# Kernel tuning notes

Hardware: AMD Instinct MI355X
Metric: run time of the kernel (lower is better)

## Reference

```python
import jax, jax.numpy as jnp
import numpy as np

NPOINT = 1024
NSAMPLE = 32
BN_EPS = 1e-5


def setup_inputs() -> dict:
    key = jax.random.key(0)
    ks = jax.random.split(key, 8)
    B, N, C = 16, 4096, 64
    chans = [C + 3, 64, 64, 128]
    d = {
        "xyz": jax.random.normal(ks[0], (B, N, 3), jnp.float32),
        "points": jax.random.normal(ks[1], (B, N, C), jnp.float32),
    }
    for i in range(3):
        d[f"w{i+1}"] = jax.random.normal(ks[2 + i], (chans[i + 1], chans[i]), jnp.float32) / np.sqrt(chans[i]).astype(np.float32)
        d[f"b{i+1}"] = jnp.zeros((chans[i + 1],), jnp.float32)
        d[f"g{i+1}"] = jnp.ones((chans[i + 1],), jnp.float32)
        d[f"be{i+1}"] = jnp.zeros((chans[i + 1],), jnp.float32)
    return d


def farthest_point_sample(xyz, npoint):
    # xyz: [B, N, 3] -> centroids: [B, npoint] int32 (deterministic start at index 0)
    B, N, _ = xyz.shape

    def step(carry, _):
        distance, farthest = carry
        centroid = jnp.take_along_axis(xyz, farthest[:, None, None], axis=1)  # [B,1,3]
        dist = jnp.sum((xyz - centroid) ** 2, axis=-1)                         # [B,N]
        distance = jnp.minimum(distance, dist)
        new_far = jnp.argmax(distance, axis=-1).astype(jnp.int32)
        return (distance, new_far), farthest

    init = (jnp.full((B, N), 1e10, xyz.dtype), jnp.zeros((B,), jnp.int32))
    _, cents = jax.lax.scan(step, init, None, length=npoint)  # [npoint, B]
    return cents.T  # [B, npoint]


def index_points(points, idx):
    # points: [B,N,C], idx: [B,...] -> [B,...,C]
    return jax.vmap(lambda p, i: p[i])(points, idx)


def bn_relu(h, g, be):
    # training-mode BatchNorm over all axes except channel (last), biased var
    m = h.mean(axis=(0, 1, 2), keepdims=True)
    v = h.var(axis=(0, 1, 2), keepdims=True)
    return jax.nn.relu((h - m) / jnp.sqrt(v + BN_EPS) * g + be)


def reference(xyz, points, w1, b1, g1, be1, w2, b2, g2, be2, w3, b3, g3, be3):
    # --- sample_and_group ---
    fps_idx = farthest_point_sample(xyz, NPOINT)           # [B,S]
    new_xyz = index_points(xyz, fps_idx)                   # [B,S,3]
    # query_ball_point in source ignores radius: kNN via argsort of sq dists
    sqrdists = jnp.sum((new_xyz[:, :, None, :] - xyz[:, None, :, :]) ** 2, axis=-1)  # [B,S,N]
    _, group_idx = jax.lax.top_k(-sqrdists, NSAMPLE)       # [B,S,K] smallest distances
    grouped_xyz = index_points(xyz, group_idx) - new_xyz[:, :, None, :]  # [B,S,K,3]
    grouped_pts = index_points(points, group_idx)          # [B,S,K,C]
    new_points = jnp.concatenate([grouped_xyz, grouped_pts], axis=-1)    # [B,S,K,C+3]
    # --- shared MLP (1x1 conv + BN + ReLU) x3, channel-last layout ---
    h = bn_relu(jnp.einsum("bskc,oc->bsko", new_points, w1) + b1, g1, be1)
    h = bn_relu(jnp.einsum("bskc,oc->bsko", h, w2) + b2, g2, be2)
    h = bn_relu(jnp.einsum("bskc,oc->bsko", h, w3) + b3, g3, be3)
    # max-pool over the neighbor (nsample) axis
    out = jnp.max(h, axis=2)  # [B,S,128]
    return (new_xyz, out)
```

## Files before the change

kernel.cpp:

```cpp
#include <hip/hip_runtime.h>
#include <cstdint>

#define NB   16
#define NPT  4096
#define CINP 64
#define SP   1024
#define KNB  32
#define NROWS (NB*SP*KNB)
#define NT_F  524288.0f
#define NBLK12 4096
#define NBLK3  8192

typedef float v2f __attribute__((ext_vector_type(2)));

__device__ __forceinline__ float sqdist3(float ax, float ay, float az,
                                         float bx, float by, float bz) {
  float dx = ax - bx, dy = ay - by, dz = az - bz;
  return __fadd_rn(__fadd_rn(__fmul_rn(dx, dx), __fmul_rn(dy, dy)), __fmul_rn(dz, dz));
}

#define DPP_STAGE_MAXF(v, ctrl)                                                   \
  do {                                                                            \
    int _t = __builtin_amdgcn_update_dpp(0, __float_as_int(v), ctrl, 0xf, 0xf, false); \
    v = fmaxf(v, __int_as_float(_t));                                             \
  } while (0)

__device__ __forceinline__ float wave_max_f32(float v) {
  DPP_STAGE_MAXF(v, 0x111);
  DPP_STAGE_MAXF(v, 0x112);
  DPP_STAGE_MAXF(v, 0x114);
  DPP_STAGE_MAXF(v, 0x118);
  DPP_STAGE_MAXF(v, 0x142);
  DPP_STAGE_MAXF(v, 0x143);
  return __int_as_float(__builtin_amdgcn_readlane(__float_as_int(v), 63));
}

#define DPP_STAGE_MINU(v, ctrl)                                                   \
  do {                                                                            \
    unsigned _t = (unsigned)__builtin_amdgcn_update_dpp(                          \
        (int)0xFFFFFFFF, (int)(v), ctrl, 0xf, 0xf, false);                        \
    v = (v < _t) ? v : _t;                                                        \
  } while (0)

__device__ __forceinline__ unsigned wave_min_u32(unsigned v) {
  DPP_STAGE_MINU(v, 0x111);
  DPP_STAGE_MINU(v, 0x112);
  DPP_STAGE_MINU(v, 0x114);
  DPP_STAGE_MINU(v, 0x118);
  DPP_STAGE_MINU(v, 0x142);
  DPP_STAGE_MINU(v, 0x143);
  return (unsigned)__builtin_amdgcn_readlane((int)v, 63);
}

#define DPP_STAGE_ADDI(v, ctrl)                                                   \
  do {                                                                            \
    int _t = __builtin_amdgcn_update_dpp(0, (v), ctrl, 0xf, 0xf, false);          \
    v += _t;                                                                      \
  } while (0)

__device__ __forceinline__ int wave_sum_i32(int v) {
  DPP_STAGE_ADDI(v, 0x111);
  DPP_STAGE_ADDI(v, 0x112);
  DPP_STAGE_ADDI(v, 0x114);
  DPP_STAGE_ADDI(v, 0x118);
  DPP_STAGE_ADDI(v, 0x142);
  DPP_STAGE_ADDI(v, 0x143);
  return __builtin_amdgcn_readlane(v, 63);
}

__global__ __launch_bounds__(256) void fps_kernel(const float* __restrict__ xyz,
                                                  float* __restrict__ newxyz) {
#pragma clang fp contract(off)
  const int b = blockIdx.x, t = threadIdx.x;
  __shared__ __align__(16) float s4[NPT * 4];
  __shared__ unsigned long long s_red[2][4];
  const float* gx = xyz + b * NPT * 3;
  for (int i = t; i < NPT * 3; i += 256) s4[(i / 3) * 4 + (i % 3)] = gx[i];
  __syncthreads();
  v2f px[8], py[8], pz[8], dst[8];
#pragma unroll
  for (int k = 0; k < 8; ++k) {
    float4 a = *(const float4*)&s4[(t + (2 * k) * 256) * 4];
    float4 c = *(const float4*)&s4[(t + (2 * k + 1) * 256) * 4];
    px[k].x = a.x; px[k].y = c.x;
    py[k].x = a.y; py[k].y = c.y;
    pz[k].x = a.z; pz[k].y = c.z;
    dst[k].x = 1e10f; dst[k].y = 1e10f;
  }
  float cx = s4[0], cy = s4[1], cz = s4[2];
  const int w = t >> 6;
  int buf = 0;
  for (int it = 0; it < SP; ++it) {
    if (t == 0) {
      float* o = newxyz + (b * SP + it) * 3;
      o[0] = cx; o[1] = cy; o[2] = cz;
    }
    v2f vcx; vcx.x = cx; vcx.y = cx;
    v2f vcy; vcy.x = cy; vcy.y = cy;
    v2f vcz; vcz.x = cz; vcz.y = cz;
    float bd = -1.0f; int bi = 0;
#pragma unroll
    for (int k = 0; k < 8; ++k) {
      v2f dx = px[k] - vcx;
      v2f dy = py[k] - vcy;
      v2f dz = pz[k] - vcz;
      v2f dd = (dx * dx + dy * dy) + dz * dz;
      float n0 = fminf(dst[k].x, dd.x);
      float n1 = fminf(dst[k].y, dd.y);
      dst[k].x = n0; dst[k].y = n1;
      if (n0 > bd) { bd = n0; bi = t + (2 * k) * 256; }
      if (n1 > bd) { bd = n1; bi = t + (2 * k + 1) * 256; }
    }
    float dw = wave_max_f32(bd);
    unsigned cand = (bd == dw) ? (unsigned)bi : 0xFFFFFFFFu;
    unsigned iw = wave_min_u32(cand);
    if ((t & 63) == 0)
      s_red[buf][w] = ((unsigned long long)__float_as_uint(dw) << 32) | (4095u - iw);
    __syncthreads();
    unsigned long long k0 = s_red[buf][0], k1 = s_red[buf][1];
    unsigned long long k2 = s_red[buf][2], k3 = s_red[buf][3];
    unsigned long long ka = k0 > k1 ? k0 : k1;
    unsigned long long kb = k2 > k3 ? k2 : k3;
    unsigned long long km = ka > kb ? ka : kb;
    int p = 4095 - (int)(km & 0xFFFFFFFFull);
    float4 cc = *(const float4*)&s4[p * 4];
    cx = cc.x; cy = cc.y; cz = cc.z;
    buf ^= 1;
  }
}

__global__ __launch_bounds__(256) void knn_kernel(const float* __restrict__ xyz,
                                                  const float* __restrict__ newxyz,
                                                  int* __restrict__ gidx) {
  const int t = threadIdx.x, lane = t & 63, w = t >> 6;
  const int q = blockIdx.x * 4 + w;
  const int b = q >> 10;
  const float* nx = newxyz + q * 3;
  const float qx = nx[0], qy = nx[1], qz = nx[2];
  const float* xb = xyz + b * NPT * 3;
  float d[64];
#pragma unroll
  for (int j = 0; j < 64; ++j) {
    int p = j * 64 + lane;
    d[j] = sqdist3(xb[p * 3], xb[p * 3 + 1], xb[p * 3 + 2], qx, qy, qz);
  }
  unsigned V = 0;
  for (int bit = 30; bit >= 0; --bit) {
    unsigned cand = V | (1u << bit);
    int c = 0;
#pragma unroll
    for (int j = 0; j < 64; ++j) c += (__float_as_uint(d[j]) < cand) ? 1 : 0;
    int ct = wave_sum_i32(c);
    if (ct < KNB) V = cand;
  }
  __shared__ int s_cnt[4], s_eqcnt[4], s_eq[4][64];
  if (lane == 0) { s_cnt[w] = 0; s_eqcnt[w] = 0; }
  __syncthreads();
  int* gout = gidx + q * KNB;
#pragma unroll
  for (int j = 0; j < 64; ++j) {
    unsigned db = __float_as_uint(d[j]);
    if (db < V) {
      int pos = atomicAdd(&s_cnt[w], 1);
      if (pos < KNB) gout[pos] = j * 64 + lane;
    } else if (db == V) {
      int pos = atomicAdd(&s_eqcnt[w], 1);
      if (pos < 64) s_eq[w][pos] = j * 64 + lane;
    }
  }
  __syncthreads();
  if (lane == 0) {
    int c1 = s_cnt[w]; if (c1 > KNB) c1 = KNB;
    int ne = s_eqcnt[w]; if (ne > 64) ne = 64;
    int need = KNB - c1;
    for (int m = 0; m < need; ++m) {
      int bi = -1, bv = 0x7fffffff;
      for (int e = 0; e < ne; ++e) {
        int v = s_eq[w][e];
        if (v < bv) { bv = v; bi = e; }
      }
      gout[c1 + m] = bv;
      if (bi >= 0) s_eq[w][bi] = 0x7fffffff;
    }
  }
}

__global__ __launch_bounds__(256) void layer1_kernel(
    const float* __restrict__ xyz, const float* __restrict__ points,
    const float* __restrict__ newxyz, const int* __restrict__ gidx,
    const float* __restrict__ w1, const float* __restrict__ b1,
    float* __restrict__ h1, float* __restrict__ part) {
  const int t = threadIdx.x, blk = blockIdx.x;
  const int R0 = blk * 128;
  const int b = R0 >> 15;
  __shared__ __align__(16) float xs[67][132];
  __shared__ __align__(16) float wsm[67][68];
  __shared__ float red[2][32][64];
  {
    int o = t & 63;
    for (int c = t >> 6; c < 67; c += 4) wsm[c][o] = w1[o * 67 + c];
  }
  {
    int r = t >> 1, q = t & 1;
    int R = R0 + r;
    int idx = gidx[R];
    if (q == 0) {
      const float* xp = xyz + (size_t)(b * NPT + idx) * 3;
      const float* nq = newxyz + (size_t)(R >> 5) * 3;
      xs[0][r] = xp[0] - nq[0];
      xs[1][r] = xp[1] - nq[1];
      xs[2][r] = xp[2] - nq[2];
    }
    const float* pp = points + (size_t)(b * NPT + idx) * CINP + q * 32;
#pragma unroll
    for (int i = 0; i < 8; ++i) {
      float4 v = *(const float4*)(pp + i * 4);
      int c = 3 + q * 32 + i * 4;
      xs[c][r] = v.x; xs[c + 1][r] = v.y; xs[c + 2][r] = v.z; xs[c + 3][r] = v.w;
    }
  }
  __syncthreads();
  const int tr = t & 31, to = t >> 5;
  float acc[4][8];
#pragma unroll
  for (int j = 0; j < 8; ++j) {
    float bb = b1[to * 8 + j];
#pragma unroll
    for (int i = 0; i < 4; ++i) acc[i][j] = bb;
  }
  for (int c = 0; c < 67; ++c) {
    float4 xv = *(const float4*)&xs[c][tr * 4];
    float4 w0 = *(const float4*)&wsm[c][to * 8];
    float4 w1v = *(const float4*)&wsm[c][to * 8 + 4];
    float xa[4] = {xv.x, xv.y, xv.z, xv.w};
    float wa[8] = {w0.x, w0.y, w0.z, w0.w, w1v.x, w1v.y, w1v.z, w1v.w};
#pragma unroll
    for (int i = 0; i < 4; ++i)
#pragma unroll
      for (int j = 0; j < 8; ++j) acc[i][j] += xa[i] * wa[j];
  }
#pragma unroll
  for (int i = 0; i < 4; ++i) {
    float4 s0; s0.x = acc[i][0]; s0.y = acc[i][1]; s0.z = acc[i][2]; s0.w = acc[i][3];
    float4 s1; s1.x = acc[i][4]; s1.y = acc[i][5]; s1.z = acc[i][6]; s1.w = acc[i][7];
    float* hp = &h1[(size_t)(R0 + tr * 4 + i) * 64 + to * 8];
    *(float4*)hp = s0;
    *(float4*)(hp + 4) = s1;
  }
#pragma unroll
  for (int j = 0; j < 8; ++j) {
    float s1 = acc[0][j] + acc[1][j] + acc[2][j] + acc[3][j];
    float s2 = acc[0][j] * acc[0][j] + acc[1][j] * acc[1][j] +
               acc[2][j] * acc[2][j] + acc[3][j] * acc[3][j];
    red[0][tr][to * 8 + j] = s1;
    red[1][tr][to * 8 + j] = s2;
  }
  __syncthreads();
  if (t < 128) {
    int stat = t >> 6, o = t & 63;
    float v = 0.f;
#pragma unroll
    for (int k = 0; k < 32; ++k) v += red[stat][k][o];
    part[(size_t)(stat * 64 + o) * NBLK12 + blk] = v;
  }
}

__global__ __launch_bounds__(256) void layer2_kernel(
    const float* __restrict__ hin, const float* __restrict__ bn,
    const float* __restrict__ w2, const float* __restrict__ b2,
    float* __restrict__ hout, float* __restrict__ part) {
  const int t = threadIdx.x, blk = blockIdx.x;
  const size_t R0 = (size_t)blk * 128;
  __shared__ __align__(16) float xs[64][132];
  __shared__ __align__(16) float wsm[64][68];
  __shared__ float red[2][32][64];
  {
    int o = t & 63;
    for (int c = t >> 6; c < 64; c += 4) wsm[c][o] = w2[o * 64 + c];
  }
  {
    int r = t >> 1, q = t & 1;
    const float* hp = hin + (R0 + r) * 64 + q * 32;
#pragma unroll
    for (int i = 0; i < 8; ++i) {
      int c = q * 32 + i * 4;
      float4 v = *(const float4*)(hp + i * 4);
      float4 sc = *(const float4*)(bn + c);
      float4 sh = *(const float4*)(bn + 64 + c);
      xs[c][r]     = fmaxf(v.x * sc.x + sh.x, 0.f);
      xs[c + 1][r] = fmaxf(v.y * sc.y + sh.y, 0.f);
      xs[c + 2][r] = fmaxf(v.z * sc.z + sh.z, 0.f);
      xs[c + 3][r] = fmaxf(v.w * sc.w + sh.w, 0.f);
    }
  }
  __syncthreads();
  const int tr = t & 31, to = t >> 5;
  float acc[4][8];
#pragma unroll
  for (int j = 0; j < 8; ++j) {
    float bb = b2[to * 8 + j];
#pragma unroll
    for (int i = 0; i < 4; ++i) acc[i][j] = bb;
  }
  for (int c = 0; c < 64; ++c) {
    float4 xv = *(const float4*)&xs[c][tr * 4];
    float4 w0 = *(const float4*)&wsm[c][to * 8];
    float4 w1v = *(const float4*)&wsm[c][to * 8 + 4];
    float xa[4] = {xv.x, xv.y, xv.z, xv.w};
    float wa[8] = {w0.x, w0.y, w0.z, w0.w, w1v.x, w1v.y, w1v.z, w1v.w};
#pragma unroll
    for (int i = 0; i < 4; ++i)
#pragma unroll
      for (int j = 0; j < 8; ++j) acc[i][j] += xa[i] * wa[j];
  }
#pragma unroll
  for (int i = 0; i < 4; ++i) {
    float4 s0; s0.x = acc[i][0]; s0.y = acc[i][1]; s0.z = acc[i][2]; s0.w = acc[i][3];
    float4 s1; s1.x = acc[i][4]; s1.y = acc[i][5]; s1.z = acc[i][6]; s1.w = acc[i][7];
    float* hp = &hout[(R0 + tr * 4 + i) * 64 + to * 8];
    *(float4*)hp = s0;
    *(float4*)(hp + 4) = s1;
  }
#pragma unroll
  for (int j = 0; j < 8; ++j) {
    float s1 = acc[0][j] + acc[1][j] + acc[2][j] + acc[3][j];
    float s2 = acc[0][j] * acc[0][j] + acc[1][j] * acc[1][j] +
               acc[2][j] * acc[2][j] + acc[3][j] * acc[3][j];
    red[0][tr][to * 8 + j] = s1;
    red[1][tr][to * 8 + j] = s2;
  }
  __syncthreads();
  if (t < 128) {
    int stat = t >> 6, o = t & 63;
    float v = 0.f;
#pragma unroll
    for (int k = 0; k < 32; ++k) v += red[stat][k][o];
    part[(size_t)(stat * 64 + o) * NBLK12 + blk] = v;
  }
}

__global__ __launch_bounds__(256) void layer3_kernel(
    const float* __restrict__ hin, const float* __restrict__ bn,
    const float* __restrict__ w3, const float* __restrict__ b3,
    float* __restrict__ maxh, float* __restrict__ minh, float* __restrict__ part) {
  const int t = threadIdx.x, blk = blockIdx.x;
  const size_t R0 = (size_t)blk * 64;
  __shared__ __align__(16) float smem[64 * 68 + 64 * 136];
  float* xs = smem;
  float* wsm = smem + 64 * 68;
  {
    int o = t & 127, q = t >> 7;
    for (int c = q; c < 64; c += 2) wsm[c * 136 + o] = w3[o * 64 + c];
  }
  {
    int r = t >> 2, q = t & 3;
    const float* hp = hin + (R0 + r) * 64 + q * 16;
#pragma unroll
    for (int i = 0; i < 4; ++i) {
      int c = q * 16 + i * 4;
      float4 v = *(const float4*)(hp + i * 4);
      float4 sc = *(const float4*)(bn + c);
      float4 sh = *(const float4*)(bn + 64 + c);
      xs[c * 68 + r]       = fmaxf(v.x * sc.x + sh.x, 0.f);
      xs[(c + 1) * 68 + r] = fmaxf(v.y * sc.y + sh.y, 0.f);
      xs[(c + 2) * 68 + r] = fmaxf(v.z * sc.z + sh.z, 0.f);
      xs[(c + 3) * 68 + r] = fmaxf(v.w * sc.w + sh.w, 0.f);
    }
  }
  __syncthreads();
  const int tr = t & 15, to = t >> 4;
  float acc[4][8];
#pragma unroll
  for (int j = 0; j < 8; ++j) {
    float bb = b3[to * 8 + j];
#pragma unroll
    for (int i = 0; i < 4; ++i) acc[i][j] = bb;
  }
  for (int c = 0; c < 64; ++c) {
    float4 xv = *(const float4*)&xs[c * 68 + tr * 4];
    float4 wv0 = *(const float4*)&wsm[c * 136 + to * 8];
    float4 wv1 = *(const float4*)&wsm[c * 136 + to * 8 + 4];
    float xa[4] = {xv.x, xv.y, xv.z, xv.w};
    float wa[8] = {wv0.x, wv0.y, wv0.z, wv0.w, wv1.x, wv1.y, wv1.z, wv1.w};
#pragma unroll
    for (int i = 0; i < 4; ++i)
#pragma unroll
      for (int j = 0; j < 8; ++j) acc[i][j] += xa[i] * wa[j];
  }
  __syncthreads();
  float* red = smem;
#pragma unroll
  for (int j = 0; j < 8; ++j) {
    float s1 = acc[0][j] + acc[1][j] + acc[2][j] + acc[3][j];
    float s2 = acc[0][j] * acc[0][j] + acc[1][j] * acc[1][j] +
               acc[2][j] * acc[2][j] + acc[3][j] * acc[3][j];
    red[(0 * 16 + tr) * 128 + to * 8 + j] = s1;
    red[(1 * 16 + tr) * 128 + to * 8 + j] = s2;
  }
  __syncthreads();
  {
    int stat = t >> 7, o = t & 127;
    float v = 0.f;
#pragma unroll
    for (int k = 0; k < 16; ++k) v += red[(stat * 16 + k) * 128 + o];
    part[(size_t)(stat * 128 + o) * NBLK3 + blk] = v;
  }
  __syncthreads();
#pragma unroll
  for (int j = 0; j < 8; ++j) {
    float mx = fmaxf(fmaxf(acc[0][j], acc[1][j]), fmaxf(acc[2][j], acc[3][j]));
    float mn = fminf(fminf(acc[0][j], acc[1][j]), fminf(acc[2][j], acc[3][j]));
    red[(0 * 16 + tr) * 128 + to * 8 + j] = mx;
    red[(1 * 16 + tr) * 128 + to * 8 + j] = mn;
  }
  __syncthreads();
  {
    int g = t >> 7, o = t & 127;
    float mx = -1e30f, mn = 1e30f;
#pragma unroll
    for (int k = 0; k < 8; ++k) {
      mx = fmaxf(mx, red[(0 * 16 + g * 8 + k) * 128 + o]);
      mn = fminf(mn, red[(1 * 16 + g * 8 + k) * 128 + o]);
    }
    size_t bs = (size_t)blk * 2 + g;
    maxh[bs * 128 + o] = mx;
    minh[bs * 128 + o] = mn;
  }
}

__global__ __launch_bounds__(256) void bn_finalize(const float* __restrict__ part,
                                                   const float* __restrict__ g,
                                                   const float* __restrict__ be,
                                                   float* __restrict__ bnout,
                                                   int Cout, int nblk) {
  const int o = blockIdx.x, t = threadIdx.x;
  float s1 = 0.f, s2 = 0.f;
  const float* p1 = part + (size_t)o * nblk;
  const float* p2 = part + (size_t)(Cout + o) * nblk;
  for (int i = t; i < nblk; i += 256) { s1 += p1[i]; s2 += p2[i]; }
#pragma unroll
  for (int off = 32; off >= 1; off >>= 1) {
    s1 += __shfl_xor(s1, off);
    s2 += __shfl_xor(s2, off);
  }
  __shared__ float r1[4], r2[4];
  if ((t & 63) == 0) { r1[t >> 6] = s1; r2[t >> 6] = s2; }
  __syncthreads();
  if (t == 0) {
    float S1 = r1[0] + r1[1] + r1[2] + r1[3];
    float S2 = r2[0] + r2[1] + r2[2] + r2[3];
    float m = S1 / NT_F;
    float v = S2 / NT_F - m * m;
    if (v < 0.f) v = 0.f;
    float inv = 1.0f / sqrtf(v + 1e-5f);
    float sc = g[o] * inv;
    bnout[o] = sc;
    bnout[Cout + o] = be[o] - m * sc;
  }
}

__global__ __launch_bounds__(256) void finalize_kernel(const float* __restrict__ maxh,
                                                       const float* __restrict__ minh,
                                                       const float* __restrict__ bn,
                                                       float* __restrict__ out2) {
  int i = blockIdx.x * 256 + threadIdx.x;
  int o = i & 127;
  float sc = bn[o], sh = bn[128 + o];
  float a = sc * maxh[i] + sh;
  float c = sc * minh[i] + sh;
  out2[i] = fmaxf(fmaxf(a, c), 0.f);
}

extern "C" void kernel_launch(void* const* d_in, const int* in_sizes, int n_in,
                              void* d_out, int out_size, void* d_ws, size_t ws_size,
                              hipStream_t stream) {
  const float* xyz = (const float*)d_in[0];
  const float* points = (const float*)d_in[1];
  const float* w1 = (const float*)d_in[2];
  const float* b1 = (const float*)d_in[3];
  const float* g1 = (const float*)d_in[4];
  const float* be1 = (const float*)d_in[5];
  const float* w2 = (const float*)d_in[6];
  const float* b2 = (const float*)d_in[7];
  const float* g2 = (const float*)d_in[8];
  const float* be2 = (const float*)d_in[9];
  const float* w3 = (const float*)d_in[10];
  const float* b3 = (const float*)d_in[11];
  const float* g3 = (const float*)d_in[12];
  const float* be3 = (const float*)d_in[13];

  float* out = (float*)d_out;
  float* newxyz = out;
  float* out2 = out + 49152;

  const size_t MiB = 1u << 20;
  char* wsb = (char*)d_ws;
  int*   gidx = (int*)wsb;
  float* h    = (float*)(wsb + 2 * MiB);
  float* part = (float*)(wsb + 130 * MiB);
  float* maxh = (float*)(wsb + 138 * MiB);
  float* minh = (float*)(wsb + 146 * MiB);
  float* bn1  = (float*)(wsb + 154 * MiB);
  float* bn2  = bn1 + 128;
  float* bn3  = bn2 + 128;

  hipLaunchKernelGGL(fps_kernel, dim3(NB), dim3(256), 0, stream, xyz, newxyz);
  hipLaunchKernelGGL(knn_kernel, dim3(16384 / 4), dim3(256), 0, stream, xyz, newxyz, gidx);
  hipLaunchKernelGGL(layer1_kernel, dim3(NBLK12), dim3(256), 0, stream,
                     xyz, points, newxyz, gidx, w1, b1, h, part);
  hipLaunchKernelGGL(bn_finalize, dim3(64), dim3(256), 0, stream, part, g1, be1, bn1, 64, NBLK12);
  hipLaunchKernelGGL(layer2_kernel, dim3(NBLK12), dim3(256), 0, stream, h, bn1, w2, b2, h, part);
  hipLaunchKernelGGL(bn_finalize, dim3(64), dim3(256), 0, stream, part, g2, be2, bn2, 64, NBLK12);
  hipLaunchKernelGGL(layer3_kernel, dim3(NBLK3), dim3(256), 0, stream,
                     h, bn2, w3, b3, maxh, minh, part);
  hipLaunchKernelGGL(bn_finalize, dim3(128), dim3(256), 0, stream, part, g3, be3, bn3, 128, NBLK3);
  hipLaunchKernelGGL(finalize_kernel, dim3(2097152 / 256), dim3(256), 0, stream,
                     maxh, minh, bn3, out2);
}
```

Before: 1.336 ms.

## Widen FPS blocks to 512 threads, defer centroid stores, pad reduction smem

The farthest-point-sampling kernel now runs 512 threads per batch with half as many points per thread, and reduces across 8 wave results instead of 4. Each selected centroid is held in a register of the thread matching its iteration and written out once after the loop, removing a global store from every iteration. The shared reduction arrays in the layer kernels get one column of padding to avoid LDS bank conflicts, and the restrict qualifiers on layer2's aliased in/out buffers are dropped. The wider FPS block shortens each thread's serial work per iteration but adds more waves to the per-iteration barrier and the cross-wave reduction.

```diff
diff --git a/kernel.cpp b/kernel.cpp
--- a/kernel.cpp
+++ b/kernel.cpp
@@ -68,39 +68,41 @@
   return __builtin_amdgcn_readlane(v, 63);
 }
 
-__global__ __launch_bounds__(256) void fps_kernel(const float* __restrict__ xyz,
+__global__ __launch_bounds__(512) void fps_kernel(const float* __restrict__ xyz,
                                                   float* __restrict__ newxyz) {
 #pragma clang fp contract(off)
   const int b = blockIdx.x, t = threadIdx.x;
   __shared__ __align__(16) float s4[NPT * 4];
-  __shared__ unsigned long long s_red[2][4];
+  __shared__ unsigned long long s_red[2][8];
   const float* gx = xyz + b * NPT * 3;
-  for (int i = t; i < NPT * 3; i += 256) s4[(i / 3) * 4 + (i % 3)] = gx[i];
-  __syncthreads();
-  v2f px[8], py[8], pz[8], dst[8];
-#pragma unroll
-  for (int k = 0; k < 8; ++k) {
-    float4 a = *(const float4*)&s4[(t + (2 * k) * 256) * 4];
-    float4 c = *(const float4*)&s4[(t + (2 * k + 1) * 256) * 4];
+  for (int i = t; i < NPT * 3; i += 512) s4[(i / 3) * 4 + (i % 3)] = gx[i];
+  __syncthreads();
+  v2f px[4], py[4], pz[4], dst[4];
+#pragma unroll
+  for (int k = 0; k < 4; ++k) {
+    float4 a = *(const float4*)&s4[(t + (2 * k) * 512) * 4];
+    float4 c = *(const float4*)&s4[(t + (2 * k + 1) * 512) * 4];
     px[k].x = a.x; px[k].y = c.x;
     py[k].x = a.y; py[k].y = c.y;
     pz[k].x = a.z; pz[k].y = c.z;
     dst[k].x = 1e10f; dst[k].y = 1e10f;
   }
   float cx = s4[0], cy = s4[1], cz = s4[2];
+  float ox0 = 0.f, oy0 = 0.f, oz0 = 0.f, ox1 = 0.f, oy1 = 0.f, oz1 = 0.f;
   const int w = t >> 6;
   int buf = 0;
   for (int it = 0; it < SP; ++it) {
-    if (t == 0) {
-      float* o = newxyz + (b * SP + it) * 3;
-      o[0] = cx; o[1] = cy; o[2] = cz;
+    if (it < 512) {
+      if (t == it) { ox0 = cx; oy0 = cy; oz0 = cz; }
+    } else {
+      if (t == it - 512) { ox1 = cx; oy1 = cy; oz1 = cz; }
     }
     v2f vcx; vcx.x = cx; vcx.y = cx;
     v2f vcy; vcy.x = cy; vcy.y = cy;
     v2f vcz; vcz.x = cz; vcz.y = cz;
     float bd = -1.0f; int bi = 0;
 #pragma unroll
-    for (int k = 0; k < 8; ++k) {
+    for (int k = 0; k < 4; ++k) {
       v2f dx = px[k] - vcx;
       v2f dy = py[k] - vcy;
       v2f dz = pz[k] - vcz;
@@ -108,8 +110,8 @@
       float n0 = fminf(dst[k].x, dd.x);
       float n1 = fminf(dst[k].y, dd.y);
       dst[k].x = n0; dst[k].y = n1;
-      if (n0 > bd) { bd = n0; bi = t + (2 * k) * 256; }
-      if (n1 > bd) { bd = n1; bi = t + (2 * k + 1) * 256; }
+      if (n0 > bd) { bd = n0; bi = t + (2 * k) * 512; }
+      if (n1 > bd) { bd = n1; bi = t + (2 * k + 1) * 512; }
     }
     float dw = wave_max_f32(bd);
     unsigned cand = (bd == dw) ? (unsigned)bi : 0xFFFFFFFFu;
@@ -119,13 +121,25 @@
     __syncthreads();
     unsigned long long k0 = s_red[buf][0], k1 = s_red[buf][1];
     unsigned long long k2 = s_red[buf][2], k3 = s_red[buf][3];
-    unsigned long long ka = k0 > k1 ? k0 : k1;
-    unsigned long long kb = k2 > k3 ? k2 : k3;
-    unsigned long long km = ka > kb ? ka : kb;
+    unsigned long long k4 = s_red[buf][4], k5 = s_red[buf][5];
+    unsigned long long k6 = s_red[buf][6], k7 = s_red[buf][7];
+    unsigned long long m0 = k0 > k1 ? k0 : k1;
+    unsigned long long m1 = k2 > k3 ? k2 : k3;
+    unsigned long long m2 = k4 > k5 ? k4 : k5;
+    unsigned long long m3 = k6 > k7 ? k6 : k7;
+    unsigned long long n0 = m0 > m1 ? m0 : m1;
+    unsigned long long n1 = m2 > m3 ? m2 : m3;
+    unsigned long long km = n0 > n1 ? n0 : n1;
     int p = 4095 - (int)(km & 0xFFFFFFFFull);
     float4 cc = *(const float4*)&s4[p * 4];
     cx = cc.x; cy = cc.y; cz = cc.z;
     buf ^= 1;
+  }
+  {
+    float* o0 = newxyz + (size_t)(b * SP + t) * 3;
+    o0[0] = ox0; o0[1] = oy0; o0[2] = oz0;
+    float* o1 = newxyz + (size_t)(b * SP + 512 + t) * 3;
+    o1[0] = ox1; o1[1] = oy1; o1[2] = oz1;
   }
 }
 
@@ -195,7 +209,7 @@
   const int b = R0 >> 15;
   __shared__ __align__(16) float xs[67][132];
   __shared__ __align__(16) float wsm[67][68];
-  __shared__ float red[2][32][64];
+  __shared__ float red[2][32][65];
   {
     int o = t & 63;
     for (int c = t >> 6; c < 67; c += 4) wsm[c][o] = w1[o * 67 + c];
@@ -266,14 +280,14 @@
 }
 
 __global__ __launch_bounds__(256) void layer2_kernel(
-    const float* __restrict__ hin, const float* __restrict__ bn,
+    const float* hin, const float* __restrict__ bn,
     const float* __restrict__ w2, const float* __restrict__ b2,
-    float* __restrict__ hout, float* __restrict__ part) {
+    float* hout, float* __restrict__ part) {
   const int t = threadIdx.x, blk = blockIdx.x;
   const size_t R0 = (size_t)blk * 128;
   __shared__ __align__(16) float xs[64][132];
   __shared__ __align__(16) float wsm[64][68];
-  __shared__ float red[2][32][64];
+  __shared__ float red[2][32][65];
   {
     int o = t & 63;
     for (int c = t >> 6; c < 64; c += 4) wsm[c][o] = w2[o * 64 + c];
@@ -394,15 +408,15 @@
     float s1 = acc[0][j] + acc[1][j] + acc[2][j] + acc[3][j];
     float s2 = acc[0][j] * acc[0][j] + acc[1][j] * acc[1][j] +
                acc[2][j] * acc[2][j] + acc[3][j] * acc[3][j];
-    red[(0 * 16 + tr) * 128 + to * 8 + j] = s1;
-    red[(1 * 16 + tr) * 128 + to * 8 + j] = s2;
+    red[(0 * 16 + tr) * 129 + to * 8 + j] = s1;
+    red[(1 * 16 + tr) * 129 + to * 8 + j] = s2;
   }
   __syncthreads();
   {
     int stat = t >> 7, o = t & 127;
     float v = 0.f;
 #pragma unroll
-    for (int k = 0; k < 16; ++k) v += red[(stat * 16 + k) * 128 + o];
+    for (int k = 0; k < 16; ++k) v += red[(stat * 16 + k) * 129 + o];
     part[(size_t)(stat * 128 + o) * NBLK3 + blk] = v;
   }
   __syncthreads();
@@ -410,8 +424,8 @@
   for (int j = 0; j < 8; ++j) {
     float mx = fmaxf(fmaxf(acc[0][j], acc[1][j]), fmaxf(acc[2][j], acc[3][j]));
     float mn = fminf(fminf(acc[0][j], acc[1][j]), fminf(acc[2][j], acc[3][j]));
-    red[(0 * 16 + tr) * 128 + to * 8 + j] = mx;
-    red[(1 * 16 + tr) * 128 + to * 8 + j] = mn;
+    red[(0 * 16 + tr) * 129 + to * 8 + j] = mx;
+    red[(1 * 16 + tr) * 129 + to * 8 + j] = mn;
   }
   __syncthreads();
   {
@@ -419,8 +433,8 @@
     float mx = -1e30f, mn = 1e30f;
 #pragma unroll
     for (int k = 0; k < 8; ++k) {
-      mx = fmaxf(mx, red[(0 * 16 + g * 8 + k) * 128 + o]);
-      mn = fminf(mn, red[(1 * 16 + g * 8 + k) * 128 + o]);
+      mx = fmaxf(mx, red[(0 * 16 + g * 8 + k) * 129 + o]);
+      mn = fminf(mn, red[(1 * 16 + g * 8 + k) * 129 + o]);
     }
     size_t bs = (size_t)blk * 2 + g;
     maxh[bs * 128 + o] = mx;
@@ -504,7 +518,7 @@
   float* bn2  = bn1 + 128;
   float* bn3  = bn2 + 128;
 
-  hipLaunchKernelGGL(fps_kernel, dim3(NB), dim3(256), 0, stream, xyz, newxyz);
+  hipLaunchKernelGGL(fps_kernel, dim3(NB), dim3(512), 0, stream, xyz, newxyz);
   hipLaunchKernelGGL(knn_kernel, dim3(16384 / 4), dim3(256), 0, stream, xyz, newxyz, gidx);
   hipLaunchKernelGGL(layer1_kernel, dim3(NBLK12), dim3(256), 0, stream,
                      xyz, points, newxyz, gidx, w1, b1, h, part);
```

Measured after the change: 1.576 ms. 17.9% more time.

## Store BN partials block-major and reduce in two stages; pad reduction smem

Applied to the files above, without the earlier changes.

The per-block BN partial sums are now written contiguously per block (row-major by block) instead of strided per channel. The old 64/128-block finalize is replaced by a 256-block coalesced first-stage reduction plus a single-block finalize. Shared reduction arrays are padded (65/129) to avoid LDS bank conflicts, and restrict is dropped on the aliased h in/out of layer2. This is meant to remove the scattered partial writes and the low-parallelism finalize, at the cost of one extra small kernel launch per layer.

```diff
diff --git a/kernel.cpp b/kernel.cpp
--- a/kernel.cpp
+++ b/kernel.cpp
@@ -195,7 +195,7 @@
   const int b = R0 >> 15;
   __shared__ __align__(16) float xs[67][132];
   __shared__ __align__(16) float wsm[67][68];
-  __shared__ float red[2][32][64];
+  __shared__ float red[2][32][65];
   {
     int o = t & 63;
     for (int c = t >> 6; c < 67; c += 4) wsm[c][o] = w1[o * 67 + c];
@@ -261,19 +261,19 @@
     float v = 0.f;
 #pragma unroll
     for (int k = 0; k < 32; ++k) v += red[stat][k][o];
-    part[(size_t)(stat * 64 + o) * NBLK12 + blk] = v;
+    part[(size_t)blk * 128 + t] = v;
   }
 }
 
 __global__ __launch_bounds__(256) void layer2_kernel(
-    const float* __restrict__ hin, const float* __restrict__ bn,
+    const float* hin, const float* __restrict__ bn,
     const float* __restrict__ w2, const float* __restrict__ b2,
-    float* __restrict__ hout, float* __restrict__ part) {
+    float* hout, float* __restrict__ part) {
   const int t = threadIdx.x, blk = blockIdx.x;
   const size_t R0 = (size_t)blk * 128;
   __shared__ __align__(16) float xs[64][132];
   __shared__ __align__(16) float wsm[64][68];
-  __shared__ float red[2][32][64];
+  __shared__ float red[2][32][65];
   {
     int o = t & 63;
     for (int c = t >> 6; c < 64; c += 4) wsm[c][o] = w2[o * 64 + c];
@@ -335,7 +335,7 @@
     float v = 0.f;
 #pragma unroll
     for (int k = 0; k < 32; ++k) v += red[stat][k][o];
-    part[(size_t)(stat * 64 + o) * NBLK12 + blk] = v;
+    part[(size_t)blk * 128 + t] = v;
   }
 }
 
@@ -394,24 +394,24 @@
     float s1 = acc[0][j] + acc[1][j] + acc[2][j] + acc[3][j];
     float s2 = acc[0][j] * acc[0][j] + acc[1][j] * acc[1][j] +
                acc[2][j] * acc[2][j] + acc[3][j] * acc[3][j];
-    red[(0 * 16 + tr) * 128 + to * 8 + j] = s1;
-    red[(1 * 16 + tr) * 128 + to * 8 + j] = s2;
+    red[(0 * 16 + tr) * 129 + to * 8 + j] = s1;
+    red[(1 * 16 + tr) * 129 + to * 8 + j] = s2;
   }
   __syncthreads();
   {
     int stat = t >> 7, o = t & 127;
     float v = 0.f;
 #pragma unroll
-    for (int k = 0; k < 16; ++k) v += red[(stat * 16 + k) * 128 + o];
-    part[(size_t)(stat * 128 + o) * NBLK3 + blk] = v;
+    for (int k = 0; k < 16; ++k) v += red[(stat * 16 + k) * 129 + o];
+    part[(size_t)blk * 256 + t] = v;
   }
   __syncthreads();
 #pragma unroll
   for (int j = 0; j < 8; ++j) {
     float mx = fmaxf(fmaxf(acc[0][j], acc[1][j]), fmaxf(acc[2][j], acc[3][j]));
     float mn = fminf(fminf(acc[0][j], acc[1][j]), fminf(acc[2][j], acc[3][j]));
-    red[(0 * 16 + tr) * 128 + to * 8 + j] = mx;
-    red[(1 * 16 + tr) * 128 + to * 8 + j] = mn;
+    red[(0 * 16 + tr) * 129 + to * 8 + j] = mx;
+    red[(1 * 16 + tr) * 129 + to * 8 + j] = mn;
   }
   __syncthreads();
   {
@@ -419,8 +419,8 @@
     float mx = -1e30f, mn = 1e30f;
 #pragma unroll
     for (int k = 0; k < 8; ++k) {
-      mx = fmaxf(mx, red[(0 * 16 + g * 8 + k) * 128 + o]);
-      mn = fminf(mn, red[(1 * 16 + g * 8 + k) * 128 + o]);
+      mx = fmaxf(mx, red[(0 * 16 + g * 8 + k) * 129 + o]);
+      mn = fminf(mn, red[(1 * 16 + g * 8 + k) * 129 + o]);
     }
     size_t bs = (size_t)blk * 2 + g;
     maxh[bs * 128 + o] = mx;
@@ -428,34 +428,53 @@
   }
 }
 
-__global__ __launch_bounds__(256) void bn_finalize(const float* __restrict__ part,
-                                                   const float* __restrict__ g,
-                                                   const float* __restrict__ be,
-                                                   float* __restrict__ bnout,
-                                                   int Cout, int nblk) {
-  const int o = blockIdx.x, t = threadIdx.x;
-  float s1 = 0.f, s2 = 0.f;
-  const float* p1 = part + (size_t)o * nblk;
-  const float* p2 = part + (size_t)(Cout + o) * nblk;
-  for (int i = t; i < nblk; i += 256) { s1 += p1[i]; s2 += p2[i]; }
-#pragma unroll
-  for (int off = 32; off >= 1; off >>= 1) {
-    s1 += __shfl_xor(s1, off);
-    s2 += __shfl_xor(s2, off);
-  }
-  __shared__ float r1[4], r2[4];
-  if ((t & 63) == 0) { r1[t >> 6] = s1; r2[t >> 6] = s2; }
-  __syncthreads();
-  if (t == 0) {
-    float S1 = r1[0] + r1[1] + r1[2] + r1[3];
-    float S2 = r2[0] + r2[1] + r2[2] + r2[3];
+__global__ __launch_bounds__(256) void stats_stage1(const float* __restrict__ in,
+                                                    float* __restrict__ out,
+                                                    int nblk, int row) {
+  const int b = blockIdx.x, t = threadIdx.x;
+  const int chunk = nblk >> 8;
+  if (row == 256) {
+    const float* p = in + (size_t)b * chunk * 256 + t;
+    float acc = 0.f;
+    for (int r = 0; r < chunk; ++r) acc += p[(size_t)r * 256];
+    out[(size_t)b * 256 + t] = acc;
+  } else {
+    __shared__ float sred[2][128];
+    const int col = t & 127, half = t >> 7;
+    const int h = chunk >> 1;
+    const float* p = in + ((size_t)b * chunk + (size_t)half * h) * 128 + col;
+    float acc = 0.f;
+    for (int r = 0; r < h; ++r) acc += p[(size_t)r * 128];
+    sred[half][col] = acc;
+    __syncthreads();
+    if (t < 128) out[(size_t)b * 128 + t] = sred[0][t] + sred[1][t];
+  }
+}
+
+__global__ __launch_bounds__(256) void bn_finalize2(const float* __restrict__ in,
+                                                    const float* __restrict__ g,
+                                                    const float* __restrict__ be,
+                                                    float* __restrict__ bnout, int Cout) {
+  const int t = threadIdx.x;
+  const int row = 2 * Cout;
+  __shared__ float ssum[256];
+  float acc = 0.f;
+  if (t < row) {
+    const float* p = in + t;
+    for (int r = 0; r < 256; ++r) acc += p[(size_t)r * row];
+  }
+  ssum[t] = acc;
+  __syncthreads();
+  if (t < Cout) {
+    float S1 = ssum[t];
+    float S2 = ssum[Cout + t];
     float m = S1 / NT_F;
     float v = S2 / NT_F - m * m;
     if (v < 0.f) v = 0.f;
     float inv = 1.0f / sqrtf(v + 1e-5f);
-    float sc = g[o] * inv;
-    bnout[o] = sc;
-    bnout[Cout + o] = be[o] - m * sc;
+    float sc = g[t] * inv;
+    bnout[t] = sc;
+    bnout[Cout + t] = be[t] - m * sc;
   }
 }
 
@@ -495,25 +514,29 @@
 
   const size_t MiB = 1u << 20;
   char* wsb = (char*)d_ws;
-  int*   gidx = (int*)wsb;
-  float* h    = (float*)(wsb + 2 * MiB);
-  float* part = (float*)(wsb + 130 * MiB);
-  float* maxh = (float*)(wsb + 138 * MiB);
-  float* minh = (float*)(wsb + 146 * MiB);
-  float* bn1  = (float*)(wsb + 154 * MiB);
-  float* bn2  = bn1 + 128;
-  float* bn3  = bn2 + 128;
+  int*   gidx  = (int*)wsb;
+  float* s1out = (float*)wsb;
+  float* bn1   = (float*)(wsb + 1 * MiB);
+  float* bn2   = bn1 + 256;
+  float* bn3   = bn2 + 256;
+  float* h     = (float*)(wsb + 2 * MiB);
+  float* part  = (float*)(wsb + 130 * MiB);
+  float* maxh  = (float*)(wsb + 138 * MiB);
+  float* minh  = (float*)(wsb + 146 * MiB);
 
   hipLaunchKernelGGL(fps_kernel, dim3(NB), dim3(256), 0, stream, xyz, newxyz);
   hipLaunchKernelGGL(knn_kernel, dim3(16384 / 4), dim3(256), 0, stream, xyz, newxyz, gidx);
   hipLaunchKernelGGL(layer1_kernel, dim3(NBLK12), dim3(256), 0, stream,
                      xyz, points, newxyz, gidx, w1, b1, h, part);
-  hipLaunchKernelGGL(bn_finalize, dim3(64), dim3(256), 0, stream, part, g1, be1, bn1, 64, NBLK12);
+  hipLaunchKernelGGL(stats_stage1, dim3(256), dim3(256), 0, stream, part, s1out, NBLK12, 128);
+  hipLaunchKernelGGL(bn_finalize2, dim3(1), dim3(256), 0, stream, s1out, g1, be1, bn1, 64);
   hipLaunchKernelGGL(layer2_kernel, dim3(NBLK12), dim3(256), 0, stream, h, bn1, w2, b2, h, part);
-  hipLaunchKernelGGL(bn_finalize, dim3(64), dim3(256), 0, stream, part, g2, be2, bn2, 64, NBLK12);
+  hipLaunchKernelGGL(stats_stage1, dim3(256), dim3(256), 0, stream, part, s1out, NBLK12, 128);
+  hipLaunchKernelGGL(bn_finalize2, dim3(1), dim3(256), 0, stream, s1out, g2, be2, bn2, 64);
   hipLaunchKernelGGL(layer3_kernel, dim3(NBLK3), dim3(256), 0, stream,
                      h, bn2, w3, b3, maxh, minh, part);
-  hipLaunchKernelGGL(bn_finalize, dim3(128), dim3(256), 0, stream, part, g3, be3, bn3, 128, NBLK3);
+  hipLaunchKernelGGL(stats_stage1, dim3(256), dim3(256), 0, stream, part, s1out, NBLK3, 256);
+  hipLaunchKernelGGL(bn_finalize2, dim3(1), dim3(256), 0, stream, s1out, g3, be3, bn3, 128);
   hipLaunchKernelGGL(finalize_kernel, dim3(2097152 / 256), dim3(256), 0, stream,
                      maxh, minh, bn3, out2);
 }
```

Measured after the change: 1.352 ms. About the same (+1.2%).
